# Kernel optimization log

Measured on AMD Instinct MI355X. Metric: run time of the kernel, lower is better.

The kernel has to match this reference:

```python
import jax, jax.numpy as jnp
import numpy as np

B, S, D, H, DFF, E = 8, 1024, 1024, 16, 4096, 16
T = B * S
C = (2 * T) // E  # top-2 capacity, capacity_factor_eff = 1.0
EPS = 1.1920929e-07


def setup_inputs() -> dict:
    key = jax.random.key(0)
    ks = jax.random.split(key, 16)
    r = lambda k, shape, sc: jax.random.normal(k, shape, dtype=jnp.float32) * sc
    return {
        "x": r(ks[0], (B, S, D), 1.0),
        "in_proj_w": r(ks[1], (3 * D, D), 0.02),
        "in_proj_b": jnp.zeros((3 * D,), jnp.float32),
        "out_proj_w": r(ks[2], (D, D), 0.02),
        "out_proj_b": jnp.zeros((D,), jnp.float32),
        "ln1_g": jnp.ones((D,), jnp.float32),
        "ln1_b": jnp.zeros((D,), jnp.float32),
        "ln2_g": jnp.ones((D,), jnp.float32),
        "ln2_b": jnp.zeros((D,), jnp.float32),
        "wg": r(ks[3], (D, E), 0.02),
        "w1": r(ks[4], (E, D, DFF), 0.02),
        "b1": jnp.zeros((E, DFF), jnp.float32),
        "w2": r(ks[5], (E, DFF, D), 0.02),
        "b2": jnp.zeros((E, D), jnp.float32),
    }


def _layernorm(v, g, b):
    m = v.mean(-1, keepdims=True)
    var = ((v - m) ** 2).mean(-1, keepdims=True)
    return (v - m) * jax.lax.rsqrt(var + 1e-5) * g + b


def reference(x, in_proj_w, in_proj_b, out_proj_w, out_proj_b,
              ln1_g, ln1_b, ln2_g, ln2_b, wg, w1, b1, w2, b2):
    hd = D // H
    # ---- self-attention block (dropout=0, eval) ----
    qkv = x @ in_proj_w.T + in_proj_b          # [B,S,3D]
    q, k, v = jnp.split(qkv, 3, axis=-1)
    heads = lambda t: t.reshape(B, S, H, hd).transpose(0, 2, 1, 3)  # [B,H,S,hd]
    q, k, v = heads(q), heads(k), heads(v)
    att = jax.nn.softmax(jnp.einsum('bhqd,bhkd->bhqk', q, k) / np.float32(np.sqrt(hd)), axis=-1)
    o = jnp.einsum('bhqk,bhkd->bhqd', att, v).transpose(0, 2, 1, 3).reshape(B, S, D)
    o = o @ out_proj_w.T + out_proj_b
    x = _layernorm(x + o, ln1_g, ln1_b)
    # ---- top-2 MoE (GShard/deepspeed-style gating, no noise at eval) ----
    xt = x.reshape(T, D)
    logits = xt @ wg                                    # [T,E]
    gates = jax.nn.softmax(logits, axis=-1)
    idx1 = jnp.argmax(gates, axis=-1)
    m1 = jax.nn.one_hot(idx1, E, dtype=jnp.float32)
    logits2 = jnp.where(m1 > 0, -jnp.inf, logits)
    idx2 = jnp.argmax(logits2, axis=-1)
    m2 = jax.nn.one_hot(idx2, E, dtype=jnp.float32)
    loc1 = jnp.cumsum(m1, axis=0) - m1                  # position within expert for top-1
    loc2 = jnp.cumsum(m2, axis=0) - m2 + m1.sum(0, keepdims=True)
    m1 = m1 * (loc1 < C)                                # drop tokens over capacity
    m2 = m2 * (loc2 < C)
    p1 = (loc1 * m1).sum(-1).astype(jnp.int32)          # [T] capacity slot
    p2 = (loc2 * m2).sum(-1).astype(jnp.int32)
    g1 = (gates * m1).sum(-1)
    g2 = (gates * m2).sum(-1)
    denom = jnp.maximum(g1 + g2, EPS)
    g1, g2 = g1 / denom, g2 / denom
    keep1 = m1.sum(-1)                                  # 1.0 if kept else 0.0
    keep2 = m2.sum(-1)
    # dispatch: scatter tokens into [E, C, D] expert buffers
    buf = jnp.zeros((E, C, D), x.dtype)
    buf = buf.at[idx1, p1].add(xt * keep1[:, None]).at[idx2, p2].add(xt * keep2[:, None])
    # grouped expert FFN
    h = jax.nn.relu(jnp.einsum('ecd,edh->ech', buf, w1) + b1[:, None, :])
    y = jnp.einsum('ech,ehd->ecd', h, w2) + b2[:, None, :]
    # combine: gather back and weight by normalized gates (zero if dropped)
    moe_out = (g1 * keep1)[:, None] * y[idx1, p1] + (g2 * keep2)[:, None] * y[idx2, p2]
    x = _layernorm(x + moe_out.reshape(B, S, D), ln2_g, ln2_b)
    return x
```

## Files before the change

kernel.cpp:

```cpp
#include <hip/hip_runtime.h>
#include <cstdint>

#define DEVI __device__ __forceinline__

typedef short short8 __attribute__((ext_vector_type(8)));
typedef float f32x4 __attribute__((ext_vector_type(4)));
typedef unsigned short u16;
typedef u16 u16x4 __attribute__((ext_vector_type(4)));

static constexpr int Bz = 8, Ss = 1024, Dd = 1024, Hh = 16, HD = 64, DFF = 4096, Ee = 16;
static constexpr int Tt = Bz * Ss;
static constexpr int Cap = (2 * Tt) / Ee;
static constexpr int D3 = 3 * Dd;
static constexpr float EPSc = 1.1920929e-07f;
static constexpr size_t PT = (size_t)Tt * Dd;

DEVI u16 f2b(float f) {
    union { float f; uint32_t u; } v; v.f = f;
    return (u16)((v.u + 0x7FFFu + ((v.u >> 16) & 1u)) >> 16);
}
DEVI float b2f(u16 h) {
    union { uint32_t u; float f; } v; v.u = ((uint32_t)h) << 16; return v.f;
}
DEVI f32x4 zf4() { f32x4 v; v[0] = 0.f; v[1] = 0.f; v[2] = 0.f; v[3] = 0.f; return v; }

DEVI void gl16(const u16* g, u16* l) {
    __builtin_amdgcn_global_load_lds(
        (const __attribute__((address_space(1))) void*)g,
        (__attribute__((address_space(3))) void*)l, 16, 0, 0);
}

DEVI int swzb(int row, int col) {
    int byte = (row * 64 + col) * 2;
    byte ^= (row & 7) << 4;
    return byte >> 1;
}

__global__ __launch_bounds__(256)
void split3_kernel(const float* __restrict__ in, u16* __restrict__ out, long long n) {
    const long long i = ((long long)blockIdx.x * 256 + threadIdx.x) * 4;
    if (i >= n) return;
    const float4 v = *(const float4*)(in + i);
    const float f[4] = {v.x, v.y, v.z, v.w};
    u16x4 ph, pm, pl;
#pragma unroll
    for (int c = 0; c < 4; ++c) {
        const u16 hi = f2b(f[c]);
        const float r1 = f[c] - b2f(hi);
        const u16 mi = f2b(r1);
        const float r2 = r1 - b2f(mi);
        const u16 lo = f2b(r2);
        ph[c] = hi; pm[c] = mi; pl[c] = lo;
    }
    *(u16x4*)(out + i) = ph;
    *(u16x4*)(out + n + i) = pm;
    *(u16x4*)(out + 2 * n + i) = pl;
}

__global__ __launch_bounds__(256)
void tconv64_kernel(const float* __restrict__ in, u16* __restrict__ out, int R, int Cc) {
    __shared__ u16 tile[64][68];
    const int z = blockIdx.z;
    const int r0 = blockIdx.y * 64, c0 = blockIdx.x * 64;
    const int tr = threadIdx.x >> 4;
    const int tc4 = (threadIdx.x & 15) * 4;
    const float* ip = in + (size_t)z * R * Cc;
#pragma unroll
    for (int i = 0; i < 4; ++i) {
        const int row = tr + i * 16;
        const float4 v = *(const float4*)(ip + (size_t)(r0 + row) * Cc + c0 + tc4);
        u16x4 w;
        w[0] = f2b(v.x); w[1] = f2b(v.y); w[2] = f2b(v.z); w[3] = f2b(v.w);
        *(u16x4*)(&tile[row][tc4]) = w;
    }
    __syncthreads();
    u16* op = out + (size_t)z * R * Cc;
#pragma unroll
    for (int i = 0; i < 4; ++i) {
        const int orow = tr + i * 16;
        u16x4 w;
#pragma unroll
        for (int j = 0; j < 4; ++j) w[j] = tile[tc4 + j][orow];
        *(u16x4*)(op + (size_t)(c0 + orow) * R + r0 + tc4) = w;
    }
}

__global__ __launch_bounds__(256)
void vtrans_kernel(const u16* __restrict__ vh, const u16* __restrict__ vl,
                   u16* __restrict__ vth, u16* __restrict__ vtl) {
    __shared__ u16 th[32][33], tl[32][33];
    const int bh = blockIdx.z, d0 = blockIdx.y * 32, s0 = blockIdx.x * 32;
    const int bb = bh >> 4, hh = bh & 15;
    const int tr = threadIdx.x >> 5, tc = threadIdx.x & 31;
#pragma unroll
    for (int i = 0; i < 4; ++i) {
        const size_t src = (size_t)(bb * Ss + s0 + tr + i * 8) * Dd + hh * HD + d0 + tc;
        th[tr + i * 8][tc] = vh[src];
        tl[tr + i * 8][tc] = vl[src];
    }
    __syncthreads();
#pragma unroll
    for (int i = 0; i < 4; ++i) {
        const size_t dst = ((size_t)bh * HD + d0 + tr + i * 8) * Ss + s0 + tc;
        vth[dst] = th[tc][tr + i * 8];
        vtl[dst] = tl[tc][tr + i * 8];
    }
}

template <int MODE>
__global__ __launch_bounds__(512)
void gemm_x3(const u16* __restrict__ A, const u16* __restrict__ Bt, void* __restrict__ Cout,
             const float* __restrict__ bias, int M, int N, int K,
             size_t psA, size_t psB,
             u16* __restrict__ qh, u16* __restrict__ ql,
             u16* __restrict__ kh, u16* __restrict__ kl,
             u16* __restrict__ vh, u16* __restrict__ vl) {
    __shared__ u16 lds[2 * 3 * 2 * 128 * 32];
    const int tid = threadIdx.x, lane = tid & 63, wid = tid >> 6;
    const int wm = wid >> 1, wn = wid & 1;
    const int lr = lane & 15, lg = lane >> 4;
    const int m0 = blockIdx.y * 128, n0 = blockIdx.x * 128;

    const u16* gsrc[6];
    int ldof[6];
#pragma unroll
    for (int c = 0; c < 6; ++c) {
        const int g = wid * 6 + c;
        const int p = g >> 4, r = g & 15, mat = r >> 3, seg = r & 7;
        const int row = seg * 16 + (lane >> 2);
        const int col = (lane & 3) * 8;
        gsrc[c] = (mat ? Bt + p * psB + (size_t)(n0 + row) * K
                       : A + p * psA + (size_t)(m0 + row) * K) + col;
        ldof[c] = (p * 2 + mat) * 4096 + seg * 512 + lane * 8;
    }

    f32x4 acc[2][4];
#pragma unroll
    for (int i = 0; i < 2; ++i)
#pragma unroll
        for (int j = 0; j < 4; ++j) acc[i][j] = zf4();

#define STAGE_X3(b, kto)                                                       \
    {                                                                          \
        _Pragma("unroll")                                                      \
        for (int c = 0; c < 6; ++c)                                            \
            gl16(gsrc[c] + (kto), lds + (b) * 24576 + ldof[c]);                \
    }

#define COMPUTE_X3(b)                                                          \
    {                                                                          \
        const u16* L = lds + (b) * 24576;                                      \
        short8 af[3][2];                                                       \
        _Pragma("unroll")                                                      \
        for (int p = 0; p < 3; ++p)                                            \
            _Pragma("unroll")                                                  \
            for (int i = 0; i < 2; ++i)                                        \
                af[p][i] = *(const short8*)(L + (p * 2) * 4096 +               \
                                            (wm * 32 + i * 16 + lr) * 32 + lg * 8); \
        _Pragma("unroll")                                                      \
        for (int bp = 0; bp < 3; ++bp) {                                       \
            short8 bf[4];                                                      \
            _Pragma("unroll")                                                  \
            for (int j = 0; j < 4; ++j)                                        \
                bf[j] = *(const short8*)(L + (bp * 2 + 1) * 4096 +             \
                                         (wn * 64 + j * 16 + lr) * 32 + lg * 8); \
            _Pragma("unroll")                                                  \
            for (int ap = 0; ap + bp < 3; ++ap)                                \
                _Pragma("unroll")                                              \
                for (int i = 0; i < 2; ++i)                                    \
                    _Pragma("unroll")                                          \
                    for (int j = 0; j < 4; ++j)                                \
                        acc[i][j] = __builtin_amdgcn_mfma_f32_16x16x32_bf16(   \
                            af[ap][i], bf[j], acc[i][j], 0, 0, 0);             \
        }                                                                      \
    }

    const int nt = K >> 5;
    STAGE_X3(0, 0)
    for (int t = 0; t < nt - 1; ++t) {
        const int cur = t & 1;
        STAGE_X3(cur ^ 1, (t + 1) * 32)
        asm volatile("s_waitcnt vmcnt(6)" ::: "memory");
        __builtin_amdgcn_s_barrier();
        COMPUTE_X3(cur)
        asm volatile("s_waitcnt lgkmcnt(0)" ::: "memory");
        __builtin_amdgcn_s_barrier();
    }
    asm volatile("s_waitcnt vmcnt(0)" ::: "memory");
    __builtin_amdgcn_s_barrier();
    COMPUTE_X3((nt - 1) & 1)

#undef STAGE_X3
#undef COMPUTE_X3

    const int r4 = lg * 4;
    const int region = n0 >> 10;
#pragma unroll
    for (int j = 0; j < 4; ++j) {
        const int col = n0 + wn * 64 + j * 16 + lr;
        const float bv = bias[col];
#pragma unroll
        for (int i = 0; i < 2; ++i) {
#pragma unroll
            for (int r = 0; r < 4; ++r) {
                const int rowg = m0 + wm * 32 + i * 16 + r4 + r;
                float v = acc[i][j][r] + bv;
                if (MODE == 2) {
                    ((float*)Cout)[(size_t)rowg * N + col] = v;
                } else {
                    const size_t off = (size_t)rowg * Dd + (col & 1023);
                    if (region == 0) {
                        const float fs = v * 0.125f;
                        const u16 h = f2b(fs);
                        qh[off] = h; ql[off] = f2b(fs - b2f(h));
                    } else if (region == 1) {
                        const u16 h = f2b(v);
                        kh[off] = h; kl[off] = f2b(v - b2f(h));
                    } else {
                        const u16 h = f2b(v);
                        vh[off] = h; vl[off] = f2b(v - b2f(h));
                    }
                }
            }
        }
    }
}

template <int RELU>
__global__ __launch_bounds__(512)
void gemm_x2(const u16* __restrict__ A, const u16* __restrict__ Bt, u16* __restrict__ Cout,
             const float* __restrict__ bias, int M, int N, int K,
             size_t sA, size_t sB, size_t sC, int sBias) {
    __shared__ u16 lds[2][2][256 * 64];
    const int tid = threadIdx.x, lane = tid & 63, wid = tid >> 6;
    const int wm = wid >> 2, wn = wid & 3;
    const int lr = lane & 15, lg = lane >> 4;
    const int m0 = blockIdx.y * 256, n0 = blockIdx.x * 256;
    const int e = blockIdx.z;
    const u16* Ab = A + (size_t)e * sA;
    const u16* Bb = Bt + (size_t)e * sB;

    const int srow = wid * 8 + (lane >> 3);
    const int scol = (lane & 7) * 8;

    f32x4 acc[8][4];
#pragma unroll
    for (int i = 0; i < 8; ++i)
#pragma unroll
        for (int j = 0; j < 4; ++j) acc[i][j] = zf4();

#define STAGE_X2(b, kt)                                                              \
    {                                                                                \
        _Pragma("unroll")                                                            \
        for (int c = 0; c < 4; ++c)                                                  \
            gl16(Ab + (size_t)(m0 + c * 64 + srow) * K + (kt) + scol,                \
                 &lds[b][0][(c * 64 + srow) * 64 + scol]);                           \
        _Pragma("unroll")                                                            \
        for (int c = 0; c < 4; ++c)                                                  \
            gl16(Bb + (size_t)(n0 + c * 64 + srow) * K + (kt) + scol,                \
                 &lds[b][1][(c * 64 + srow) * 64 + scol]);                           \
    }

#define COMPUTE_X2(b)                                                                \
    {                                                                                \
        _Pragma("unroll")                                                            \
        for (int ks = 0; ks < 2; ++ks) {                                             \
            short8 af[8], bf[4];                                                     \
            _Pragma("unroll")                                                        \
            for (int i = 0; i < 8; ++i)                                              \
                af[i] = *(const short8*)(&lds[b][0][(wm * 128 + i * 16 + lr) * 64 + ks * 32 + lg * 8]); \
            _Pragma("unroll")                                                        \
            for (int j = 0; j < 4; ++j)                                              \
                bf[j] = *(const short8*)(&lds[b][1][(wn * 64 + j * 16 + lr) * 64 + ks * 32 + lg * 8]);  \
            _Pragma("unroll")                                                        \
            for (int i = 0; i < 8; ++i)                                              \
                _Pragma("unroll")                                                    \
                for (int j = 0; j < 4; ++j)                                          \
                    acc[i][j] = __builtin_amdgcn_mfma_f32_16x16x32_bf16(af[i], bf[j], acc[i][j], 0, 0, 0); \
        }                                                                            \
    }

    const int nt = K >> 6;
    STAGE_X2(0, 0)
    for (int t = 0; t < nt - 1; ++t) {
        const int cur = t & 1;
        STAGE_X2(cur ^ 1, (t + 1) * 64)
        asm volatile("s_waitcnt vmcnt(8)" ::: "memory");
        __builtin_amdgcn_s_barrier();
        COMPUTE_X2(cur)
        asm volatile("s_waitcnt lgkmcnt(0)" ::: "memory");
        __builtin_amdgcn_s_barrier();
    }
    asm volatile("s_waitcnt vmcnt(0)" ::: "memory");
    __builtin_amdgcn_s_barrier();
    COMPUTE_X2((nt - 1) & 1)

#undef STAGE_X2
#undef COMPUTE_X2

    const int r4 = lg * 4;
#pragma unroll
    for (int j = 0; j < 4; ++j) {
        const int col = n0 + wn * 64 + j * 16 + lr;
        const float bv = bias[(size_t)e * sBias + col];
#pragma unroll
        for (int i = 0; i < 8; ++i) {
#pragma unroll
            for (int r = 0; r < 4; ++r) {
                const int rowg = m0 + wm * 128 + i * 16 + r4 + r;
                float v = acc[i][j][r] + bv;
                if (RELU) v = fmaxf(v, 0.f);
                Cout[(size_t)e * sC + (size_t)rowg * N + col] = f2b(v);
            }
        }
    }
}

__global__ __launch_bounds__(256)
void attn_mfma(const u16* __restrict__ qhp, const u16* __restrict__ qlp,
               const u16* __restrict__ khp, const u16* __restrict__ klp,
               const u16* __restrict__ vthp, const u16* __restrict__ vtlp,
               u16* __restrict__ os) {
    __shared__ u16 Khi[64 * 64], Klo[64 * 64];
    __shared__ u16 Vhi[64 * 64], Vlo[64 * 64];
    __shared__ u16 Phi[4][16 * 64], Plo[4][16 * 64];

    const int qt = blockIdx.x, bh = blockIdx.y;
    const int bb = bh >> 4, hh = bh & 15;
    const int tid = threadIdx.x, lane = tid & 63, wid = tid >> 6;
    const int lr = lane & 15, lg = lane >> 4;

    short8 qhi[2], qlo[2];
    {
        const size_t qbase = (size_t)(bb * Ss + qt * 64 + wid * 16 + lr) * Dd + hh * HD;
#pragma unroll
        for (int ks = 0; ks < 2; ++ks) {
            qhi[ks] = *(const short8*)(qhp + qbase + ks * 32 + lg * 8);
            qlo[ks] = *(const short8*)(qlp + qbase + ks * 32 + lg * 8);
        }
    }

    float mrun[4], lrun[4];
    f32x4 oacc[4];
#pragma unroll
    for (int r = 0; r < 4; ++r) { mrun[r] = -1e30f; lrun[r] = 0.f; }
#pragma unroll
    for (int nf = 0; nf < 4; ++nf) oacc[nf] = zf4();

    const int srow = tid >> 2;
    const int sd = (tid & 3) * 16;

    u16* const PhiW = Phi[wid];
    u16* const PloW = Plo[wid];

    for (int kt = 0; kt < Ss / 64; ++kt) {
        const size_t krow = (size_t)(bb * Ss + kt * 64 + srow) * Dd + hh * HD + sd;
        const short8 k0 = *(const short8*)(khp + krow);
        const short8 k1 = *(const short8*)(khp + krow + 8);
        const short8 l0 = *(const short8*)(klp + krow);
        const short8 l1 = *(const short8*)(klp + krow + 8);
        const size_t vrow = ((size_t)bh * HD + srow) * Ss + kt * 64 + sd;
        const short8 v0 = *(const short8*)(vthp + vrow);
        const short8 v1 = *(const short8*)(vthp + vrow + 8);
        const short8 w0 = *(const short8*)(vtlp + vrow);
        const short8 w1 = *(const short8*)(vtlp + vrow + 8);
        __syncthreads();
        *(short8*)(Khi + swzb(srow, sd)) = k0;
        *(short8*)(Khi + swzb(srow, sd + 8)) = k1;
        *(short8*)(Klo + swzb(srow, sd)) = l0;
        *(short8*)(Klo + swzb(srow, sd + 8)) = l1;
        *(short8*)(Vhi + swzb(srow, sd)) = v0;
        *(short8*)(Vhi + swzb(srow, sd + 8)) = v1;
        *(short8*)(Vlo + swzb(srow, sd)) = w0;
        *(short8*)(Vlo + swzb(srow, sd + 8)) = w1;
        __syncthreads();

        f32x4 sc[4];
#pragma unroll
        for (int nf = 0; nf < 4; ++nf) sc[nf] = zf4();
#pragma unroll
        for (int nf = 0; nf < 4; ++nf)
#pragma unroll
            for (int ks = 0; ks < 2; ++ks) {
                const short8 kh = *(const short8*)(Khi + swzb(nf * 16 + lr, ks * 32 + lg * 8));
                const short8 kl = *(const short8*)(Klo + swzb(nf * 16 + lr, ks * 32 + lg * 8));
                sc[nf] = __builtin_amdgcn_mfma_f32_16x16x32_bf16(qhi[ks], kh, sc[nf], 0, 0, 0);
                sc[nf] = __builtin_amdgcn_mfma_f32_16x16x32_bf16(qhi[ks], kl, sc[nf], 0, 0, 0);
                sc[nf] = __builtin_amdgcn_mfma_f32_16x16x32_bf16(qlo[ks], kh, sc[nf], 0, 0, 0);
                sc[nf] = __builtin_amdgcn_mfma_f32_16x16x32_bf16(qlo[ks], kl, sc[nf], 0, 0, 0);
            }

        float scl[4];
#pragma unroll
        for (int r = 0; r < 4; ++r) {
            float m = fmaxf(fmaxf(sc[0][r], sc[1][r]), fmaxf(sc[2][r], sc[3][r]));
            m = fmaxf(m, __shfl_xor(m, 1));
            m = fmaxf(m, __shfl_xor(m, 2));
            m = fmaxf(m, __shfl_xor(m, 4));
            m = fmaxf(m, __shfl_xor(m, 8));
            const float mn = fmaxf(mrun[r], m);
            scl[r] = __expf(mrun[r] - mn);
            mrun[r] = mn;
            float s = 0.f;
#pragma unroll
            for (int nf = 0; nf < 4; ++nf) {
                const float p = __expf(sc[nf][r] - mn);
                sc[nf][r] = p;
                s += p;
            }
            s += __shfl_xor(s, 1);
            s += __shfl_xor(s, 2);
            s += __shfl_xor(s, 4);
            s += __shfl_xor(s, 8);
            lrun[r] = lrun[r] * scl[r] + s;
        }

#pragma unroll
        for (int nf = 0; nf < 4; ++nf)
#pragma unroll
            for (int r = 0; r < 4; ++r) {
                const float p = sc[nf][r];
                const u16 h = f2b(p);
                const int idx = swzb(lg * 4 + r, nf * 16 + lr);
                PhiW[idx] = h;
                PloW[idx] = f2b(p - b2f(h));
            }

#pragma unroll
        for (int nf = 0; nf < 4; ++nf)
#pragma unroll
            for (int r = 0; r < 4; ++r) oacc[nf][r] *= scl[r];

#pragma unroll
        for (int ks = 0; ks < 2; ++ks) {
            const short8 ph = *(const short8*)(PhiW + swzb(lr, ks * 32 + lg * 8));
            const short8 pl = *(const short8*)(PloW + swzb(lr, ks * 32 + lg * 8));
#pragma unroll
            for (int nf = 0; nf < 4; ++nf) {
                const short8 vh = *(const short8*)(Vhi + swzb(nf * 16 + lr, ks * 32 + lg * 8));
                const short8 vl = *(const short8*)(Vlo + swzb(nf * 16 + lr, ks * 32 + lg * 8));
                oacc[nf] = __builtin_amdgcn_mfma_f32_16x16x32_bf16(ph, vh, oacc[nf], 0, 0, 0);
                oacc[nf] = __builtin_amdgcn_mfma_f32_16x16x32_bf16(ph, vl, oacc[nf], 0, 0, 0);
                oacc[nf] = __builtin_amdgcn_mfma_f32_16x16x32_bf16(pl, vh, oacc[nf], 0, 0, 0);
                oacc[nf] = __builtin_amdgcn_mfma_f32_16x16x32_bf16(pl, vl, oacc[nf], 0, 0, 0);
            }
        }
    }

#pragma unroll
    for (int r = 0; r < 4; ++r) {
        const float inv = 1.f / lrun[r];
        const size_t base = (size_t)(bb * Ss + qt * 64 + wid * 16 + lg * 4 + r) * Dd + hh * HD;
#pragma unroll
        for (int nf = 0; nf < 4; ++nf) {
            const float o = oacc[nf][r] * inv;
            const u16 h = f2b(o);
            const float r1 = o - b2f(h);
            const u16 m = f2b(r1);
            const u16 l = f2b(r1 - b2f(m));
            const size_t off = base + nf * 16 + lr;
            os[off] = h;
            os[PT + off] = m;
            os[2 * PT + off] = l;
        }
    }
}

DEVI double block_reduce_d(double v, double* sred, int tid) {
#pragma unroll
    for (int off = 32; off > 0; off >>= 1) v += __shfl_down(v, off);
    __syncthreads();
    if ((tid & 63) == 0) sred[tid >> 6] = v;
    __syncthreads();
    return sred[0] + sred[1] + sred[2] + sred[3];
}

__global__ __launch_bounds__(256)
void ln1_kernel(const float* __restrict__ x, const float* __restrict__ ap,
                const float* __restrict__ g, const float* __restrict__ b,
                float* __restrict__ x1f) {
    __shared__ double sred[4];
    const int t = blockIdx.x, tid = threadIdx.x;
    const float4 xv = ((const float4*)(x + (size_t)t * Dd))[tid];
    const float4 av = ((const float4*)(ap + (size_t)t * Dd))[tid];
    const double v0 = (double)xv.x + (double)av.x;
    const double v1 = (double)xv.y + (double)av.y;
    const double v2 = (double)xv.z + (double)av.z;
    const double v3 = (double)xv.w + (double)av.w;
    const double s = block_reduce_d(v0 + v1 + v2 + v3, sred, tid);
    const double mean = s * (1.0 / Dd);
    const double c0 = v0 - mean, c1 = v1 - mean, c2 = v2 - mean, c3 = v3 - mean;
    const double s2 = block_reduce_d(c0 * c0 + c1 * c1 + c2 * c2 + c3 * c3, sred, tid);
    const double rstd = 1.0 / sqrt(s2 * (1.0 / Dd) + 1e-5);
    const float4 gv = ((const float4*)g)[tid];
    const float4 bv = ((const float4*)b)[tid];
    float4 ov;
    ov.x = (float)(c0 * rstd * (double)gv.x + (double)bv.x);
    ov.y = (float)(c1 * rstd * (double)gv.y + (double)bv.y);
    ov.z = (float)(c2 * rstd * (double)gv.z + (double)bv.z);
    ov.w = (float)(c3 * rstd * (double)gv.w + (double)bv.w);
    ((float4*)(x1f + (size_t)t * Dd))[tid] = ov;
}

__global__ __launch_bounds__(256)
void gate1_kernel(const float* __restrict__ x1f, const float* __restrict__ wg,
                  int* __restrict__ idx1, int* __restrict__ idx2,
                  float* __restrict__ gate1, float* __restrict__ gate2) {
    const int tid = threadIdx.x, lane = tid & 63, wid = tid >> 6;
    const int t = blockIdx.x * 4 + wid;
    double acc[16];
#pragma unroll
    for (int e = 0; e < 16; ++e) acc[e] = 0.0;
    for (int i = 0; i < 16; ++i) {
        const int d = i * 64 + lane;
        const double xv = (double)x1f[(size_t)t * Dd + d];
        const float4* wr = (const float4*)(wg + (size_t)d * 16);
        const float4 w0 = wr[0], w1 = wr[1], w2 = wr[2], w3 = wr[3];
        acc[0] += xv * (double)w0.x;  acc[1] += xv * (double)w0.y;
        acc[2] += xv * (double)w0.z;  acc[3] += xv * (double)w0.w;
        acc[4] += xv * (double)w1.x;  acc[5] += xv * (double)w1.y;
        acc[6] += xv * (double)w1.z;  acc[7] += xv * (double)w1.w;
        acc[8] += xv * (double)w2.x;  acc[9] += xv * (double)w2.y;
        acc[10] += xv * (double)w2.z; acc[11] += xv * (double)w2.w;
        acc[12] += xv * (double)w3.x; acc[13] += xv * (double)w3.y;
        acc[14] += xv * (double)w3.z; acc[15] += xv * (double)w3.w;
    }
#pragma unroll
    for (int e = 0; e < 16; ++e) {
        acc[e] += __shfl_xor(acc[e], 1);
        acc[e] += __shfl_xor(acc[e], 2);
        acc[e] += __shfl_xor(acc[e], 4);
        acc[e] += __shfl_xor(acc[e], 8);
        acc[e] += __shfl_xor(acc[e], 16);
        acc[e] += __shfl_xor(acc[e], 32);
    }
    if (lane == 0) {
        double mx = acc[0];
#pragma unroll
        for (int e = 1; e < 16; ++e) mx = fmax(mx, acc[e]);
        double z = 0.0, ex[16];
#pragma unroll
        for (int e = 0; e < 16; ++e) { ex[e] = exp(acc[e] - mx); z += ex[e]; }
        int b1 = 0; double v1 = acc[0];
#pragma unroll
        for (int e = 1; e < 16; ++e) if (acc[e] > v1) { v1 = acc[e]; b1 = e; }
        int b2 = (b1 == 0) ? 1 : 0; double v2 = acc[b2];
#pragma unroll
        for (int e = 0; e < 16; ++e) if (e != b1 && acc[e] > v2) { v2 = acc[e]; b2 = e; }
        const double rz = 1.0 / z;
        idx1[t] = b1; idx2[t] = b2;
        gate1[t] = (float)(ex[b1] * rz); gate2[t] = (float)(ex[b2] * rz);
    }
}

__global__ __launch_bounds__(256)
void gate2_kernel(const int* __restrict__ idx1, const int* __restrict__ idx2,
                  const float* __restrict__ gate1, const float* __restrict__ gate2,
                  int* __restrict__ p1, int* __restrict__ p2,
                  int* __restrict__ k1, int* __restrict__ k2,
                  float* __restrict__ w1, float* __restrict__ w2) {
    __shared__ int hist[16];
    __shared__ unsigned long long sb1[4][16], sb2[4][16];
    __shared__ int sbase1[16], sbase2[16];
    const int tid = threadIdx.x, lane = tid & 63, wid = tid >> 6;
    if (tid < 16) hist[tid] = 0;
    __syncthreads();
    for (int t = tid; t < Tt; t += 256) atomicAdd(&hist[idx1[t]], 1);
    __syncthreads();
    if (tid < 16) { sbase1[tid] = 0; sbase2[tid] = hist[tid]; }
    __syncthreads();
    const unsigned long long below = (1ULL << lane) - 1ULL;
    for (int ch = 0; ch < Tt / 256; ++ch) {
        const int t = ch * 256 + tid;
        const int a = idx1[t], b = idx2[t];
#pragma unroll
        for (int e = 0; e < 16; ++e) {
            const unsigned long long m1 = __ballot(a == e);
            const unsigned long long m2 = __ballot(b == e);
            if (lane == 0) { sb1[wid][e] = m1; sb2[wid][e] = m2; }
        }
        __syncthreads();
        int r1 = __popcll(sb1[wid][a] & below);
        int r2 = __popcll(sb2[wid][b] & below);
#pragma unroll
        for (int w = 0; w < 4; ++w)
            if (w < wid) { r1 += __popcll(sb1[w][a]); r2 += __popcll(sb2[w][b]); }
        const int loc1 = sbase1[a] + r1, loc2 = sbase2[b] + r2;
        const int kk1 = loc1 < Cap, kk2 = loc2 < Cap;
        const float g1 = kk1 ? gate1[t] : 0.f;
        const float g2 = kk2 ? gate2[t] : 0.f;
        const float dn = fmaxf(g1 + g2, EPSc);
        p1[t] = kk1 ? loc1 : 0;
        p2[t] = kk2 ? loc2 : 0;
        k1[t] = kk1; k2[t] = kk2;
        w1[t] = g1 / dn; w2[t] = g2 / dn;
        __syncthreads();
        if (tid == 0) {
#pragma unroll
            for (int e = 0; e < 16; ++e) {
                int c1 = 0, c2 = 0;
#pragma unroll
                for (int w = 0; w < 4; ++w) { c1 += __popcll(sb1[w][e]); c2 += __popcll(sb2[w][e]); }
                sbase1[e] += c1; sbase2[e] += c2;
            }
        }
        __syncthreads();
    }
}

__global__ __launch_bounds__(256)
void dispatch_kernel(const float* __restrict__ x1f,
                     const int* __restrict__ i1, const int* __restrict__ p1, const int* __restrict__ k1,
                     const int* __restrict__ i2, const int* __restrict__ p2, const int* __restrict__ k2,
                     u16* __restrict__ buf) {
    const int t = blockIdx.x, tid = threadIdx.x;
    const float4 v = ((const float4*)(x1f + (size_t)t * Dd))[tid];
    u16x4 pw;
    pw[0] = f2b(v.x); pw[1] = f2b(v.y); pw[2] = f2b(v.z); pw[3] = f2b(v.w);
    if (k1[t]) *(u16x4*)(buf + ((size_t)i1[t] * Cap + p1[t]) * Dd + tid * 4) = pw;
    if (k2[t]) *(u16x4*)(buf + ((size_t)i2[t] * Cap + p2[t]) * Dd + tid * 4) = pw;
}

__global__ __launch_bounds__(256)
void combine_ln2(const float* __restrict__ x1f, const u16* __restrict__ y,
                 const int* __restrict__ i1, const int* __restrict__ p1, const float* __restrict__ w1,
                 const int* __restrict__ i2, const int* __restrict__ p2, const float* __restrict__ w2,
                 const float* __restrict__ g, const float* __restrict__ b,
                 float* __restrict__ out) {
    __shared__ double sred[4];
    const int t = blockIdx.x, tid = threadIdx.x;
    const size_t r1 = ((size_t)i1[t] * Cap + p1[t]) * Dd;
    const size_t r2 = ((size_t)i2[t] * Cap + p2[t]) * Dd;
    const double a1 = (double)w1[t], a2 = (double)w2[t];
    const u16x4 y1 = *(const u16x4*)(y + r1 + tid * 4);
    const u16x4 y2 = *(const u16x4*)(y + r2 + tid * 4);
    const float4 xv = ((const float4*)(x1f + (size_t)t * Dd))[tid];
    const double v0 = (double)xv.x + a1 * (double)b2f(y1[0]) + a2 * (double)b2f(y2[0]);
    const double v1 = (double)xv.y + a1 * (double)b2f(y1[1]) + a2 * (double)b2f(y2[1]);
    const double v2 = (double)xv.z + a1 * (double)b2f(y1[2]) + a2 * (double)b2f(y2[2]);
    const double v3 = (double)xv.w + a1 * (double)b2f(y1[3]) + a2 * (double)b2f(y2[3]);
    const double s = block_reduce_d(v0 + v1 + v2 + v3, sred, tid);
    const double mean = s * (1.0 / Dd);
    const double c0 = v0 - mean, c1 = v1 - mean, c2 = v2 - mean, c3 = v3 - mean;
    const double s2 = block_reduce_d(c0 * c0 + c1 * c1 + c2 * c2 + c3 * c3, sred, tid);
    const double rstd = 1.0 / sqrt(s2 * (1.0 / Dd) + 1e-5);
    const float4 gv = ((const float4*)g)[tid];
    const float4 bv = ((const float4*)b)[tid];
    float4 ov;
    ov.x = (float)(c0 * rstd * (double)gv.x + (double)bv.x);
    ov.y = (float)(c1 * rstd * (double)gv.y + (double)bv.y);
    ov.z = (float)(c2 * rstd * (double)gv.z + (double)bv.z);
    ov.w = (float)(c3 * rstd * (double)gv.w + (double)bv.w);
    ((float4*)(out + (size_t)t * Dd))[tid] = ov;
}

extern "C" void kernel_launch(void* const* d_in, const int* in_sizes, int n_in,
                              void* d_out, int out_size, void* d_ws, size_t ws_size,
                              hipStream_t stream) {
    (void)in_sizes; (void)n_in; (void)out_size; (void)ws_size;
    const float* x    = (const float*)d_in[0];
    const float* inW  = (const float*)d_in[1];
    const float* inB  = (const float*)d_in[2];
    const float* outW = (const float*)d_in[3];
    const float* outB = (const float*)d_in[4];
    const float* ln1g = (const float*)d_in[5];
    const float* ln1b = (const float*)d_in[6];
    const float* ln2g = (const float*)d_in[7];
    const float* ln2b = (const float*)d_in[8];
    const float* wg   = (const float*)d_in[9];
    const float* w1   = (const float*)d_in[10];
    const float* b1   = (const float*)d_in[11];
    const float* w2   = (const float*)d_in[12];
    const float* b2   = (const float*)d_in[13];
    float* out = (float*)d_out;

    char* ws = (char*)d_ws;
    const size_t MB = 1024 * 1024;
    u16*   xs3   = (u16*)(ws + 0);
    u16*   inW3  = (u16*)(ws + 48 * MB);
    u16*   qh    = (u16*)(ws + 66 * MB);
    u16*   ql    = (u16*)(ws + 82 * MB);
    u16*   kh    = (u16*)(ws + 98 * MB);
    u16*   kl    = (u16*)(ws + 114 * MB);
    u16*   vh    = (u16*)(ws + 130 * MB);
    u16*   vl    = (u16*)(ws + 146 * MB);
    u16*   vth   = (u16*)(ws + 162 * MB);
    u16*   vtl   = (u16*)(ws + 178 * MB);
    u16*   os3   = (u16*)(ws + 194 * MB);
    u16*   outW3 = (u16*)(ws + 0);
    float* aproj = (float*)(ws + 6 * MB);
    u16*   wt    = (u16*)(ws + 0);
    u16*   hbuf  = (u16*)(ws + 128 * MB);
    u16*   ybuf  = (u16*)(ws + 256 * MB);
    u16*   ebuf  = (u16*)(ws + 288 * MB);
    float* x1f   = (float*)(ws + 320 * MB);
    char*  gbase = ws + 352 * MB;
    int*   idx1 = (int*)(gbase + 0 * Tt * 4);
    int*   idx2 = (int*)(gbase + 1 * Tt * 4);
    float* gt1  = (float*)(gbase + 2 * Tt * 4);
    float* gt2  = (float*)(gbase + 3 * Tt * 4);
    int*   p1   = (int*)(gbase + 4 * Tt * 4);
    int*   p2   = (int*)(gbase + 5 * Tt * 4);
    int*   k1   = (int*)(gbase + 6 * Tt * 4);
    int*   k2   = (int*)(gbase + 7 * Tt * 4);
    float* w1c  = (float*)(gbase + 8 * Tt * 4);
    float* w2c  = (float*)(gbase + 9 * Tt * 4);

    const long long nTD = (long long)Tt * Dd;
    const long long nW1 = (long long)D3 * Dd;
    const long long nW2 = (long long)Dd * Dd;

    split3_kernel<<<(int)(nTD / 1024), 256, 0, stream>>>(x, xs3, nTD);
    split3_kernel<<<(int)(nW1 / 1024), 256, 0, stream>>>(inW, inW3, nW1);
    gemm_x3<3><<<dim3(D3 / 128, Tt / 128, 1), 512, 0, stream>>>(
        xs3, inW3, nullptr, inB, Tt, D3, Dd, (size_t)nTD, (size_t)nW1,
        qh, ql, kh, kl, vh, vl);
    vtrans_kernel<<<dim3(Ss / 32, HD / 32, Bz * Hh), 256, 0, stream>>>(vh, vl, vth, vtl);
    attn_mfma<<<dim3(Ss / 64, Bz * Hh), 256, 0, stream>>>(qh, ql, kh, kl, vth, vtl, os3);
    split3_kernel<<<(int)(nW2 / 1024), 256, 0, stream>>>(outW, outW3, nW2);
    gemm_x3<2><<<dim3(Dd / 128, Tt / 128, 1), 512, 0, stream>>>(
        os3, outW3, aproj, outB, Tt, Dd, Dd, (size_t)nTD, (size_t)nW2,
        nullptr, nullptr, nullptr, nullptr, nullptr, nullptr);
    ln1_kernel<<<Tt, 256, 0, stream>>>(x, aproj, ln1g, ln1b, x1f);
    gate1_kernel<<<Tt / 4, 256, 0, stream>>>(x1f, wg, idx1, idx2, gt1, gt2);
    gate2_kernel<<<1, 256, 0, stream>>>(idx1, idx2, gt1, gt2, p1, p2, k1, k2, w1c, w2c);
    hipMemsetAsync(ebuf, 0, (size_t)Ee * Cap * Dd * 2, stream);
    dispatch_kernel<<<Tt, 256, 0, stream>>>(x1f, idx1, p1, k1, idx2, p2, k2, ebuf);
    tconv64_kernel<<<dim3(DFF / 64, Dd / 64, Ee), 256, 0, stream>>>(w1, wt, Dd, DFF);
    gemm_x2<1><<<dim3(DFF / 256, Cap / 256, Ee), 512, 0, stream>>>(
        ebuf, wt, hbuf, b1, Cap, DFF, Dd,
        (size_t)Cap * Dd, (size_t)DFF * Dd, (size_t)Cap * DFF, DFF);
    tconv64_kernel<<<dim3(Dd / 64, DFF / 64, Ee), 256, 0, stream>>>(w2, wt, DFF, Dd);
    gemm_x2<0><<<dim3(Dd / 256, Cap / 256, Ee), 512, 0, stream>>>(
        hbuf, wt, ybuf, b2, Cap, Dd, DFF,
        (size_t)Cap * DFF, (size_t)Dd * DFF, (size_t)Cap * Dd, Dd);
    combine_ln2<<<Tt, 256, 0, stream>>>(x1f, ybuf, idx1, p1, w1c, idx2, p2, w2c, ln2g, ln2b, out);
}
```

Before: 1.342 ms.

## Widen split-bf16 GEMM tiles to 128x256 and swizzle LDS in expert GEMM

The split-precision (3-term bf16) GEMM used for the QKV and output projections grows its tile from 128x128 to 128x256. Warps are rearranged 2x4, each computing 64x64, so every A fragment feeds more MFMAs and global and LDS traffic per flop drops. The expert FFN GEMM gets an XOR swizzle on its LDS column index, applied to the global source column on staging and to the LDS read address, to avoid bank conflicts on the fragment reads. The larger tile uses more LDS (about 144 KB double-buffered) and more accumulator registers, so occupancy and grid parallelism drop.

```diff
diff --git a/kernel.cpp b/kernel.cpp
--- a/kernel.cpp
+++ b/kernel.cpp
@@ -109,65 +109,66 @@
 
 template <int MODE>
 __global__ __launch_bounds__(512)
-void gemm_x3(const u16* __restrict__ A, const u16* __restrict__ Bt, void* __restrict__ Cout,
-             const float* __restrict__ bias, int M, int N, int K,
-             size_t psA, size_t psB,
-             u16* __restrict__ qh, u16* __restrict__ ql,
-             u16* __restrict__ kh, u16* __restrict__ kl,
-             u16* __restrict__ vh, u16* __restrict__ vl) {
-    __shared__ u16 lds[2 * 3 * 2 * 128 * 32];
+void gemm_x3b(const u16* __restrict__ A, const u16* __restrict__ Bt, void* __restrict__ Cout,
+              const float* __restrict__ bias, int M, int N, int K,
+              size_t psA, size_t psB,
+              u16* __restrict__ qh, u16* __restrict__ ql,
+              u16* __restrict__ kh, u16* __restrict__ kl,
+              u16* __restrict__ vh, u16* __restrict__ vl) {
+    __shared__ u16 lds[2 * 36864];
     const int tid = threadIdx.x, lane = tid & 63, wid = tid >> 6;
-    const int wm = wid >> 1, wn = wid & 1;
+    const int wm = wid >> 2, wn = wid & 3;
     const int lr = lane & 15, lg = lane >> 4;
-    const int m0 = blockIdx.y * 128, n0 = blockIdx.x * 128;
-
-    const u16* gsrc[6];
-    int ldof[6];
-#pragma unroll
-    for (int c = 0; c < 6; ++c) {
-        const int g = wid * 6 + c;
-        const int p = g >> 4, r = g & 15, mat = r >> 3, seg = r & 7;
-        const int row = seg * 16 + (lane >> 2);
-        const int col = (lane & 3) * 8;
-        gsrc[c] = (mat ? Bt + p * psB + (size_t)(n0 + row) * K
-                       : A + p * psA + (size_t)(m0 + row) * K) + col;
-        ldof[c] = (p * 2 + mat) * 4096 + seg * 512 + lane * 8;
-    }
-
-    f32x4 acc[2][4];
-#pragma unroll
-    for (int i = 0; i < 2; ++i)
+    const int m0 = blockIdx.y * 128, n0 = blockIdx.x * 256;
+
+    const u16* gsrc[9];
+    int ldof[9];
+#pragma unroll
+    for (int c = 0; c < 9; ++c) {
+        const int g = wid * 9 + c;
+        int p, seg, base;
+        const u16* mat;
+        size_t rowb;
+        if (g < 24) { p = g >> 3; seg = g & 7;  mat = A;  rowb = (size_t)(m0 + seg * 16 + (lane >> 2)) * K; base = p * 4096;          mat += p * psA; }
+        else { const int gb = g - 24; p = gb >> 4; seg = gb & 15; mat = Bt; rowb = (size_t)(n0 + seg * 16 + (lane >> 2)) * K; base = 12288 + p * 8192; mat += p * psB; }
+        gsrc[c] = mat + rowb + (lane & 3) * 8;
+        ldof[c] = base + seg * 512 + lane * 8;
+    }
+
+    f32x4 acc[4][4];
+#pragma unroll
+    for (int i = 0; i < 4; ++i)
 #pragma unroll
         for (int j = 0; j < 4; ++j) acc[i][j] = zf4();
 
-#define STAGE_X3(b, kto)                                                       \
+#define STAGE_X3B(b, kto)                                                      \
     {                                                                          \
         _Pragma("unroll")                                                      \
-        for (int c = 0; c < 6; ++c)                                            \
-            gl16(gsrc[c] + (kto), lds + (b) * 24576 + ldof[c]);                \
-    }
-
-#define COMPUTE_X3(b)                                                          \
+        for (int c = 0; c < 9; ++c)                                            \
+            gl16(gsrc[c] + (kto), lds + (b) * 36864 + ldof[c]);                \
+    }
+
+#define COMPUTE_X3B(b)                                                         \
     {                                                                          \
-        const u16* L = lds + (b) * 24576;                                      \
-        short8 af[3][2];                                                       \
+        const u16* L = lds + (b) * 36864;                                      \
+        short8 af[3][4];                                                       \
         _Pragma("unroll")                                                      \
         for (int p = 0; p < 3; ++p)                                            \
             _Pragma("unroll")                                                  \
-            for (int i = 0; i < 2; ++i)                                        \
-                af[p][i] = *(const short8*)(L + (p * 2) * 4096 +               \
-                                            (wm * 32 + i * 16 + lr) * 32 + lg * 8); \
+            for (int i = 0; i < 4; ++i)                                        \
+                af[p][i] = *(const short8*)(L + p * 4096 +                     \
+                                            (wm * 64 + i * 16 + lr) * 32 + lg * 8); \
         _Pragma("unroll")                                                      \
         for (int bp = 0; bp < 3; ++bp) {                                       \
             short8 bf[4];                                                      \
             _Pragma("unroll")                                                  \
             for (int j = 0; j < 4; ++j)                                        \
-                bf[j] = *(const short8*)(L + (bp * 2 + 1) * 4096 +             \
+                bf[j] = *(const short8*)(L + 12288 + bp * 8192 +               \
                                          (wn * 64 + j * 16 + lr) * 32 + lg * 8); \
             _Pragma("unroll")                                                  \
             for (int ap = 0; ap + bp < 3; ++ap)                                \
                 _Pragma("unroll")                                              \
-                for (int i = 0; i < 2; ++i)                                    \
+                for (int i = 0; i < 4; ++i)                                    \
                     _Pragma("unroll")                                          \
                     for (int j = 0; j < 4; ++j)                                \
                         acc[i][j] = __builtin_amdgcn_mfma_f32_16x16x32_bf16(   \
@@ -176,34 +177,34 @@
     }
 
     const int nt = K >> 5;
-    STAGE_X3(0, 0)
+    STAGE_X3B(0, 0)
     for (int t = 0; t < nt - 1; ++t) {
         const int cur = t & 1;
-        STAGE_X3(cur ^ 1, (t + 1) * 32)
-        asm volatile("s_waitcnt vmcnt(6)" ::: "memory");
+        STAGE_X3B(cur ^ 1, (t + 1) * 32)
+        asm volatile("s_waitcnt vmcnt(9)" ::: "memory");
         __builtin_amdgcn_s_barrier();
-        COMPUTE_X3(cur)
+        COMPUTE_X3B(cur)
         asm volatile("s_waitcnt lgkmcnt(0)" ::: "memory");
         __builtin_amdgcn_s_barrier();
     }
     asm volatile("s_waitcnt vmcnt(0)" ::: "memory");
     __builtin_amdgcn_s_barrier();
-    COMPUTE_X3((nt - 1) & 1)
-
-#undef STAGE_X3
-#undef COMPUTE_X3
+    COMPUTE_X3B((nt - 1) & 1)
+
+#undef STAGE_X3B
+#undef COMPUTE_X3B
 
     const int r4 = lg * 4;
-    const int region = n0 >> 10;
 #pragma unroll
     for (int j = 0; j < 4; ++j) {
         const int col = n0 + wn * 64 + j * 16 + lr;
         const float bv = bias[col];
-#pragma unroll
-        for (int i = 0; i < 2; ++i) {
+        const int region = col >> 10;
+#pragma unroll
+        for (int i = 0; i < 4; ++i) {
 #pragma unroll
             for (int r = 0; r < 4; ++r) {
-                const int rowg = m0 + wm * 32 + i * 16 + r4 + r;
+                const int rowg = m0 + wm * 64 + i * 16 + r4 + r;
                 float v = acc[i][j][r] + bv;
                 if (MODE == 2) {
                     ((float*)Cout)[(size_t)rowg * N + col] = v;
@@ -241,7 +242,7 @@
     const u16* Bb = Bt + (size_t)e * sB;
 
     const int srow = wid * 8 + (lane >> 3);
-    const int scol = (lane & 7) * 8;
+    const int sscol = (((lane & 7) ^ ((lane >> 3) & 7))) * 8;
 
     f32x4 acc[8][4];
 #pragma unroll
@@ -253,12 +254,12 @@
     {                                                                                \
         _Pragma("unroll")                                                            \
         for (int c = 0; c < 4; ++c)                                                  \
-            gl16(Ab + (size_t)(m0 + c * 64 + srow) * K + (kt) + scol,                \
-                 &lds[b][0][(c * 64 + srow) * 64 + scol]);                           \
+            gl16(Ab + (size_t)(m0 + c * 64 + srow) * K + (kt) + sscol,               \
+                 &lds[b][0][(c * 64 + srow) * 64 + (lane & 7) * 8]);                 \
         _Pragma("unroll")                                                            \
         for (int c = 0; c < 4; ++c)                                                  \
-            gl16(Bb + (size_t)(n0 + c * 64 + srow) * K + (kt) + scol,                \
-                 &lds[b][1][(c * 64 + srow) * 64 + scol]);                           \
+            gl16(Bb + (size_t)(n0 + c * 64 + srow) * K + (kt) + sscol,               \
+                 &lds[b][1][(c * 64 + srow) * 64 + (lane & 7) * 8]);                 \
     }
 
 #define COMPUTE_X2(b)                                                                \
@@ -268,10 +269,12 @@
             short8 af[8], bf[4];                                                     \
             _Pragma("unroll")                                                        \
             for (int i = 0; i < 8; ++i)                                              \
-                af[i] = *(const short8*)(&lds[b][0][(wm * 128 + i * 16 + lr) * 64 + ks * 32 + lg * 8]); \
+                af[i] = *(const short8*)(&lds[b][0][(wm * 128 + i * 16 + lr) * 64 +  \
+                                                    (((ks * 4 + lg) ^ (lr & 7)) * 8)]); \
             _Pragma("unroll")                                                        \
             for (int j = 0; j < 4; ++j)                                              \
-                bf[j] = *(const short8*)(&lds[b][1][(wn * 64 + j * 16 + lr) * 64 + ks * 32 + lg * 8]);  \
+                bf[j] = *(const short8*)(&lds[b][1][(wn * 64 + j * 16 + lr) * 64 +   \
+                                                    (((ks * 4 + lg) ^ (lr & 7)) * 8)]); \
             _Pragma("unroll")                                                        \
             for (int i = 0; i < 8; ++i)                                              \
                 _Pragma("unroll")                                                    \
@@ -712,13 +715,13 @@
 
     split3_kernel<<<(int)(nTD / 1024), 256, 0, stream>>>(x, xs3, nTD);
     split3_kernel<<<(int)(nW1 / 1024), 256, 0, stream>>>(inW, inW3, nW1);
-    gemm_x3<3><<<dim3(D3 / 128, Tt / 128, 1), 512, 0, stream>>>(
+    gemm_x3b<3><<<dim3(D3 / 256, Tt / 128, 1), 512, 0, stream>>>(
         xs3, inW3, nullptr, inB, Tt, D3, Dd, (size_t)nTD, (size_t)nW1,
         qh, ql, kh, kl, vh, vl);
     vtrans_kernel<<<dim3(Ss / 32, HD / 32, Bz * Hh), 256, 0, stream>>>(vh, vl, vth, vtl);
     attn_mfma<<<dim3(Ss / 64, Bz * Hh), 256, 0, stream>>>(qh, ql, kh, kl, vth, vtl, os3);
     split3_kernel<<<(int)(nW2 / 1024), 256, 0, stream>>>(outW, outW3, nW2);
-    gemm_x3<2><<<dim3(Dd / 128, Tt / 128, 1), 512, 0, stream>>>(
+    gemm_x3b<2><<<dim3(Dd / 256, Tt / 128, 1), 512, 0, stream>>>(
         os3, outW3, aproj, outB, Tt, Dd, Dd, (size_t)nTD, (size_t)nW2,
         nullptr, nullptr, nullptr, nullptr, nullptr, nullptr);
     ln1_kernel<<<Tt, 256, 0, stream>>>(x, aproj, ln1g, ln1b, x1f);
```

After: 1.320 ms. Within noise of the previous version (-1.6%).
